# Kernel tuning notes

Measured on AMD Instinct MI355X. Metric: run time of the kernel, lower is better.

## Reference

```python
import jax, jax.numpy as jnp
import numpy as np

BATCH, MAXLEN, EMBED = 32, 128, 16
N = MAXLEN * EMBED  # flattened feature dim
# row-major lower-triangular (i >= j) indices, matching tf.where on the mask
_RI, _CI = np.tril_indices(N)
_RI = jnp.asarray(_RI)
_CI = jnp.asarray(_CI)


def setup_inputs() -> dict:
    key = jax.random.key(0)
    data = jax.random.normal(key, (BATCH, MAXLEN, EMBED), dtype=jnp.float32)
    return {"data": data}


def reference(data):
    b = data.shape[0]
    flat = data.reshape(b, -1)                      # (B, N) linear features
    # lower-triangular entries of the per-sample outer product, row-major
    nonlinear = flat[:, _RI] * flat[:, _CI]         # (B, N*(N+1)/2)
    return jnp.concatenate([flat, nonlinear], axis=-1)
```

## Files before the change

kernel.cpp:

```cpp
#include <hip/hip_runtime.h>


#define BATCH      32
#define NFEAT      2048
#define TRI_COUNT  (NFEAT * (NFEAT + 1) / 2)
#define PER_BATCH  (NFEAT + TRI_COUNT)
#define PAIRS      (NFEAT / 2)

__global__ void __launch_bounds__(256)
sideways_rows_kernel(const float* __restrict__ in, float* __restrict__ out) {
    const int blk = blockIdx.x;
    const int b   = blk >> 10;
    const int p   = blk & (PAIRS - 1);
    const int t   = threadIdx.x;

    const float* __restrict__ f  = in + b * NFEAT;
    float* __restrict__       ob = out + b * PER_BATCH;

    if (p == 0) {
        for (int j = t; j < NFEAT; j += 256) ob[j] = f[j];
    }

    {
        const int   i    = p;
        const float fi   = f[i];
        float* __restrict__ orow = ob + NFEAT + ((i * (i + 1)) >> 1);
        for (int j = t; j <= i; j += 256) orow[j] = fi * f[j];
    }

    {
        const int   i    = NFEAT - 1 - p;
        const float fi   = f[i];
        float* __restrict__ orow = ob + NFEAT + ((i * (i + 1)) >> 1);
        for (int j = t; j <= i; j += 256) orow[j] = fi * f[j];
    }
}

extern "C" void kernel_launch(void* const* d_in, const int* in_sizes, int n_in,
                              void* d_out, int out_size, void* d_ws, size_t ws_size,
                              hipStream_t stream) {
    const float* in  = (const float*)d_in[0];
    float*       out = (float*)d_out;
    const int grid = BATCH * PAIRS;
    hipLaunchKernelGGL(sideways_rows_kernel, dim3(grid), dim3(256), 0, stream,
                       in, out);
}
```

Measured before the change: 46.47 us.

## Walk flattened triangle in float4 chunks instead of per-row scalar stores

Each block now takes a fixed contiguous chunk of the flattened lower-triangular output for one batch, rather than a pair of rows. Each thread recovers its starting row with a sqrt estimate and then walks rows incrementally. Every iteration writes four consecutive outputs as one float4 store, and the linear copy is also vectorised. This aims to even out work across blocks, cut the grid from 32768 to 2048 blocks, and widen stores on a bandwidth-bound write. In exchange it adds per-element row-boundary checks and gathered reads of the input row.

```diff
diff --git a/kernel.cpp b/kernel.cpp
--- a/kernel.cpp
+++ b/kernel.cpp
@@ -5,34 +5,58 @@
 #define NFEAT      2048
 #define TRI_COUNT  (NFEAT * (NFEAT + 1) / 2)
 #define PER_BATCH  (NFEAT + TRI_COUNT)
-#define PAIRS      (NFEAT / 2)
+#define TRI4       (TRI_COUNT / 4)
+#define CHUNKS     64
+#define CHUNK4     (TRI4 / CHUNKS)
+
+__device__ __forceinline__ int tri(int i) { return (i * (i + 1)) >> 1; }
 
 __global__ void __launch_bounds__(256)
-sideways_rows_kernel(const float* __restrict__ in, float* __restrict__ out) {
+sideways_walk_kernel(const float* __restrict__ in, float* __restrict__ out) {
     const int blk = blockIdx.x;
-    const int b   = blk >> 10;
-    const int p   = blk & (PAIRS - 1);
+    const int b   = blk >> 6;
+    const int c   = blk & (CHUNKS - 1);
     const int t   = threadIdx.x;
 
-    const float* __restrict__ f  = in + b * NFEAT;
-    float* __restrict__       ob = out + b * PER_BATCH;
+    const float* __restrict__ f    = in + b * NFEAT;
+    float* __restrict__       ob   = out + b * PER_BATCH;
+    float* __restrict__       otri = ob + NFEAT;
 
-    if (p == 0) {
-        for (int j = t; j < NFEAT; j += 256) ob[j] = f[j];
+    if (c == 0) {
+        for (int v = t; v < NFEAT / 4; v += 256)
+            reinterpret_cast<float4*>(ob)[v] =
+                reinterpret_cast<const float4*>(f)[v];
     }
 
-    {
-        const int   i    = p;
-        const float fi   = f[i];
-        float* __restrict__ orow = ob + NFEAT + ((i * (i + 1)) >> 1);
-        for (int j = t; j <= i; j += 256) orow[j] = fi * f[j];
-    }
+    int idx4      = c * CHUNK4 + t;
+    const int end = (c + 1) * CHUNK4;
+    int te        = idx4 << 2;
 
-    {
-        const int   i    = NFEAT - 1 - p;
-        const float fi   = f[i];
-        float* __restrict__ orow = ob + NFEAT + ((i * (i + 1)) >> 1);
-        for (int j = t; j <= i; j += 256) orow[j] = fi * f[j];
+    int i = (int)((sqrtf((float)(8 * te) + 1.0f) - 1.0f) * 0.5f);
+    if (i < 0) i = 0;
+    if (i > NFEAT - 1) i = NFEAT - 1;
+    while (tri(i) > te) --i;
+    while (tri(i + 1) <= te) ++i;
+    int   rowstart = tri(i);
+    float fi       = f[i];
+
+    for (; idx4 < end; idx4 += 256, te += 1024) {
+        while (rowstart + i + 1 <= te) { rowstart += i + 1; ++i; }
+        fi = f[i];
+
+        float ov[4];
+        int   rs = rowstart, ii = i;
+        float fv = fi;
+#pragma unroll
+        for (int k = 0; k < 4; ++k) {
+            const int e = te + k;
+            while (rs + ii + 1 <= e) { rs += ii + 1; ++ii; fv = f[ii]; }
+            ov[k] = fv * f[e - rs];
+        }
+        rowstart = rs; i = ii; fi = fv;
+
+        *reinterpret_cast<float4*>(otri + te) =
+            make_float4(ov[0], ov[1], ov[2], ov[3]);
     }
 }
 
@@ -41,7 +65,7 @@
                               hipStream_t stream) {
     const float* in  = (const float*)d_in[0];
     float*       out = (float*)d_out;
-    const int grid = BATCH * PAIRS;
-    hipLaunchKernelGGL(sideways_rows_kernel, dim3(grid), dim3(256), 0, stream,
+    const int grid = BATCH * CHUNKS;
+    hipLaunchKernelGGL(sideways_walk_kernel, dim3(grid), dim3(256), 0, stream,
                        in, out);
 }
```

Measured after the change: 74.38 us. 60.1% more time.
